# Performance work log

Measured on AMD Instinct MI355X. Metric: run time of the kernel, lower is better.

Reference implementation:

```python
import jax, jax.numpy as jnp
import numpy as np

N_SUPPORT = 8192
N_QUERY = 8192
INPUT_DIM = 1024
EMBED_DIM = 512
N_CLASSES = 64


def setup_inputs() -> dict:
    key = jax.random.key(0)
    k1, k2, k3, k4 = jax.random.split(key, 4)
    support_data = jax.random.normal(k1, (N_SUPPORT, INPUT_DIM), dtype=jnp.float32)
    query_data = jax.random.normal(k2, (N_QUERY, INPUT_DIM), dtype=jnp.float32)
    support_labels = jax.random.randint(k3, (N_SUPPORT,), 0, N_CLASSES, dtype=jnp.int32)
    W = jax.random.normal(k4, (INPUT_DIM, EMBED_DIM), dtype=jnp.float32) * (1.0 / np.sqrt(INPUT_DIM))
    return {"support_data": support_data, "support_labels": support_labels,
            "query_data": query_data, "W": W}


def _l2_normalize(x, eps=1e-12):
    # Matches F.normalize(p=2): x / max(||x||, eps)
    n = jnp.linalg.norm(x, axis=-1, keepdims=True)
    return x / jnp.maximum(n, eps)


def reference(support_data, support_labels, query_data, W):
    # encoder: single linear projection
    s_emb = support_data @ W            # [Ns, D]
    q_emb = query_data @ W              # [Nq, D]
    s_norm = _l2_normalize(s_emb)
    q_norm = _l2_normalize(q_emb)
    # cosine similarities for all query/support pairs: [Nq, Ns]
    sims = q_norm @ s_norm.T
    # per-class sum over support samples (torch.unique -> sorted 0..N_CLASSES-1)
    # segment_sum along the support axis: [N_classes, Nq] -> [Nq, N_classes]
    class_scores = jax.ops.segment_sum(sims.T, support_labels, num_segments=N_CLASSES).T
    return jax.nn.softmax(class_scores, axis=-1)
```

## Files before the change

### kernel.cpp

```cpp
#include <hip/hip_runtime.h>
#include <hip/hip_bf16.h>

#define NS 8192
#define NQ 8192
#define NTOT 16384
#define KDIM 1024
#define ED 512
#define NC 64

typedef __attribute__((ext_vector_type(4))) float fx4;
typedef __attribute__((ext_vector_type(8))) short sx8;
typedef __attribute__((ext_vector_type(8))) unsigned short ux8;

__device__ __forceinline__ unsigned short f2bf(float f) {
  union { float f; unsigned u; } v; v.f = f;
  unsigned r = v.u + 0x7fffu + ((v.u >> 16) & 1u);
  return (unsigned short)(r >> 16);
}
__device__ __forceinline__ float bf2f(unsigned short h) {
  union { unsigned u; float f; } v; v.u = ((unsigned)h) << 16;
  return v.f;
}

__global__ __launch_bounds__(256) void k_prep(
    const float* __restrict__ W, unsigned short* __restrict__ Wtp,
    float* __restrict__ rowssq, float* __restrict__ Pacc) {
  int c = blockIdx.x * 256 + threadIdx.x;
  int lane = c & 63;
  int j    = (c >> 6) & 3;
  int s2   = (c >> 8) & 1;
  int kt   = (c >> 9) & 15;
  int n64  = c >> 13;
  int quad = lane >> 4, ml = lane & 15;
  int n  = n64 * 64 + j * 16 + ml;
  int kb = kt * 64 + (s2 * 4 + quad) * 8;
  ux8 o;
#pragma unroll
  for (int e = 0; e < 8; ++e) o[e] = f2bf(W[(size_t)(kb + e) * ED + n]);
  *(ux8*)&Wtp[(size_t)c * 8] = o;
  if (c < NTOT) rowssq[c] = 0.f;
  if (c < NC * ED) Pacc[c] = 0.f;
}

__global__ __launch_bounds__(256, 4) void k_gemm_embed(
    const float* __restrict__ Xs, const float* __restrict__ Xq,
    const unsigned short* __restrict__ Wtp,
    unsigned short* __restrict__ emb, float* __restrict__ rowssq) {
  __shared__ unsigned short Ash[2][64 * 8 * 8];

  int lid = blockIdx.x;
  int x = lid & 7;
  int s = lid >> 3;
  int m_blk = x * 32 + (s >> 2);
  int n_blk = s & 3;

  const float* Xsrc = (m_blk < 128)
      ? (Xs + (size_t)m_blk * 64 * KDIM)
      : (Xq + (size_t)(m_blk - 128) * 64 * KDIM);

  int t = threadIdx.x;
  int lane = t & 63, w = t >> 6;
  int quad = lane >> 4, ml = lane & 15;
  int n64 = n_blk * 2 + (w >> 1);
  int jb = (w & 1) * 2;

  const unsigned short* Bbase = Wtp + ((size_t)n64 * 8192 + lane) * 8;

  fx4 acc[4][2];
#pragma unroll
  for (int i = 0; i < 4; ++i)
#pragma unroll
    for (int j = 0; j < 2; ++j) acc[i][j] = fx4{0.f, 0.f, 0.f, 0.f};

  fx4 avA[2][2], avB[2][2];

  auto loadA = [&](int kt, fx4 (&av)[2][2]) {
    int k0 = kt * 64;
#pragma unroll
    for (int c = 0; c < 2; ++c) {
      int ch = t + 256 * c;
      int m = ch >> 3, kq = ch & 7;
      const float* g = &Xsrc[(size_t)m * KDIM + k0 + kq * 8];
      av[c][0] = *(const fx4*)g;
      av[c][1] = *(const fx4*)(g + 4);
    }
  };
  auto writeA = [&](const fx4 (&av)[2][2], int bbuf) {
#pragma unroll
    for (int c = 0; c < 2; ++c) {
      int ch = t + 256 * c;
      int m = ch >> 3, kq = ch & 7;
      ux8 o;
      o[0] = f2bf(av[c][0].x); o[1] = f2bf(av[c][0].y);
      o[2] = f2bf(av[c][0].z); o[3] = f2bf(av[c][0].w);
      o[4] = f2bf(av[c][1].x); o[5] = f2bf(av[c][1].y);
      o[6] = f2bf(av[c][1].z); o[7] = f2bf(av[c][1].w);
      *(ux8*)&Ash[bbuf][((m * 8) + (kq ^ (m & 7))) * 8] = o;
    }
  };
  auto loadB = [&](int kt, sx8 (&bf)[2][2]) {
#pragma unroll
    for (int s2 = 0; s2 < 2; ++s2)
#pragma unroll
      for (int j = 0; j < 2; ++j)
        bf[s2][j] = *(const sx8*)&Bbase[(size_t)(kt * 512 + s2 * 256 + (jb + j) * 64) * 8];
  };
  auto compute = [&](int b, const sx8 (&bf)[2][2]) {
#pragma unroll
    for (int s2 = 0; s2 < 2; ++s2) {
      int kq = s2 * 4 + quad;
      sx8 af[4];
#pragma unroll
      for (int i = 0; i < 4; ++i) {
        int row = i * 16 + ml;
        af[i] = *(const sx8*)&Ash[b][(row * 8 + (kq ^ (row & 7))) * 8];
      }
#pragma unroll
      for (int i = 0; i < 4; ++i)
#pragma unroll
        for (int j = 0; j < 2; ++j)
          acc[i][j] = __builtin_amdgcn_mfma_f32_16x16x32_bf16(af[i], bf[s2][j], acc[i][j], 0, 0, 0);
    }
  };
  auto sync_step = [&]() {
    __builtin_amdgcn_sched_barrier(0);
    asm volatile("s_waitcnt lgkmcnt(0)" ::: "memory");
    __builtin_amdgcn_s_barrier();
    __builtin_amdgcn_sched_barrier(0);
  };

  loadA(0, avA);
  loadA(1, avB);
  writeA(avA, 0);
  sync_step();

  for (int it = 0; it < 8; ++it) {
    int kt0 = it * 2;
    sx8 bf[2][2];
    loadB(kt0, bf);
    loadA(kt0 + 2 < 16 ? kt0 + 2 : 15, avA);
    compute(0, bf);
    writeA(avB, 1);
    sync_step();

    loadB(kt0 + 1, bf);
    loadA(kt0 + 3 < 16 ? kt0 + 3 : 15, avB);
    compute(1, bf);
    writeA(avA, 0);
    sync_step();
  }

  int grow = m_blk * 64;
  int gcol = n_blk * 128 + w * 32;
#pragma unroll
  for (int i = 0; i < 4; ++i) {
#pragma unroll
    for (int r = 0; r < 4; ++r) {
      int mrow = grow + i * 16 + quad * 4 + r;
      float p = 0.f;
#pragma unroll
      for (int j = 0; j < 2; ++j) {
        emb[(size_t)mrow * ED + gcol + j * 16 + ml] = f2bf(acc[i][j][r]);
        p += acc[i][j][r] * acc[i][j][r];
      }
#pragma unroll
      for (int off = 1; off < 16; off <<= 1) p += __shfl_xor(p, off, 16);
      if (ml == 0) atomicAdd(&rowssq[mrow], p);
    }
  }
}

__global__ __launch_bounds__(256) void k_proto(
    const unsigned short* __restrict__ embS, const float* __restrict__ rowssq,
    const int* __restrict__ labels, float* __restrict__ Pacc) {
  __shared__ float Pl[NC * 64];
  int t = threadIdx.x;
#pragma unroll
  for (int i = 0; i < 16; ++i) Pl[i * 256 + t] = 0.f;
  __syncthreads();

  int w = t >> 6, lane = t & 63;
  int ds = blockIdx.y;
  int row0 = blockIdx.x * 256;
#pragma unroll 4
  for (int r = w; r < 256; r += 4) {
    int row = row0 + r;
    int lbl = labels[row];
    float scale = 1.0f / fmaxf(sqrtf(rowssq[row]), 1e-12f);
    float v = bf2f(embS[(size_t)row * ED + ds * 64 + lane]) * scale;
    atomicAdd(&Pl[lbl * 64 + lane], v);
  }
  __syncthreads();

#pragma unroll
  for (int i = 0; i < 16; ++i) {
    int idx = i * 256 + t;
    atomicAdd(&Pacc[(size_t)(idx >> 6) * ED + ds * 64 + (idx & 63)], Pl[idx]);
  }
}

__global__ __launch_bounds__(64) void k_scores(
    const unsigned short* __restrict__ embQ, const float* __restrict__ ssqQ,
    const float* __restrict__ Pacc, float* __restrict__ out) {
  int lane = threadIdx.x;
  int quad = lane >> 4, ml = lane & 15;
  int qrow0 = blockIdx.x * 16;

  fx4 acc[4];
#pragma unroll
  for (int i = 0; i < 4; ++i) acc[i] = fx4{0.f, 0.f, 0.f, 0.f};

#pragma unroll 4
  for (int ki = 0; ki < 16; ++ki) {
    sx8 a = *(const sx8*)&embQ[(size_t)(qrow0 + ml) * ED + ki * 32 + quad * 8];
    int d0 = ki * 32 + quad * 8;
#pragma unroll
    for (int nt = 0; nt < 4; ++nt) {
      const float* Prow = &Pacc[(size_t)(nt * 16 + ml) * ED + d0];
      fx4 p0 = *(const fx4*)Prow;
      fx4 p1 = *(const fx4*)(Prow + 4);
      ux8 bb;
      bb[0] = f2bf(p0.x); bb[1] = f2bf(p0.y); bb[2] = f2bf(p0.z); bb[3] = f2bf(p0.w);
      bb[4] = f2bf(p1.x); bb[5] = f2bf(p1.y); bb[6] = f2bf(p1.z); bb[7] = f2bf(p1.w);
      acc[nt] = __builtin_amdgcn_mfma_f32_16x16x32_bf16(a, *(sx8*)&bb, acc[nt], 0, 0, 0);
    }
  }

#pragma unroll
  for (int r = 0; r < 4; ++r) {
    int qq = qrow0 + quad * 4 + r;
    float scale = 1.0f / fmaxf(sqrtf(ssqQ[qq]), 1e-12f);
    float s[4];
#pragma unroll
    for (int nt = 0; nt < 4; ++nt) s[nt] = acc[nt][r] * scale;
    float m = fmaxf(fmaxf(s[0], s[1]), fmaxf(s[2], s[3]));
#pragma unroll
    for (int off = 1; off < 16; off <<= 1) m = fmaxf(m, __shfl_xor(m, off, 16));
    float e[4], ssum = 0.f;
#pragma unroll
    for (int nt = 0; nt < 4; ++nt) { e[nt] = __expf(s[nt] - m); ssum += e[nt]; }
#pragma unroll
    for (int off = 1; off < 16; off <<= 1) ssum += __shfl_xor(ssum, off, 16);
    float inv = 1.0f / ssum;
#pragma unroll
    for (int nt = 0; nt < 4; ++nt)
      out[(size_t)qq * NC + nt * 16 + ml] = e[nt] * inv;
  }
}

extern "C" void kernel_launch(void* const* d_in, const int* in_sizes, int n_in,
                              void* d_out, int out_size, void* d_ws, size_t ws_size,
                              hipStream_t stream) {
  const float* Xs     = (const float*)d_in[0];
  const int*   labels = (const int*)d_in[1];
  const float* Xq     = (const float*)d_in[2];
  const float* W      = (const float*)d_in[3];
  float* out = (float*)d_out;

  char* ws = (char*)d_ws;
  size_t off = 0;
  unsigned short* Wtp = (unsigned short*)(ws + off); off += (size_t)ED * KDIM * 2;
  unsigned short* emb = (unsigned short*)(ws + off); off += (size_t)NTOT * ED * 2;
  float* rowssq = (float*)(ws + off); off += (size_t)NTOT * 4;
  float* Pacc   = (float*)(ws + off); off += (size_t)NC * ED * 4;

  k_prep<<<256, 256, 0, stream>>>(W, Wtp, rowssq, Pacc);
  k_gemm_embed<<<1024, 256, 0, stream>>>(Xs, Xq, Wtp, emb, rowssq);
  k_proto<<<dim3(32, 8), 256, 0, stream>>>(emb, rowssq, labels, Pacc);
  k_scores<<<NQ / 16, 64, 0, stream>>>(emb + (size_t)NS * ED, rowssq + NS, Pacc, out);
}
```

Before: 173.4 us.

## Prefetch B fragments one step ahead and stage bf16 prototypes in LDS

The embedding GEMM now double-buffers the W fragments in registers, loading the next k-tile's B operands before computing the current one so their global latency overlaps the MFMAs. The scores kernel grows to 256-thread blocks of 64 queries. Each block converts the fp32 prototype matrix to bf16 once into a 64 KB shared-memory layout, so waves no longer reload and reconvert it from global memory for every query tile. The costs are extra VGPRs in the GEMM and heavy LDS use in the scores kernel, which can limit occupancy.

```diff
diff --git a/kernel.cpp b/kernel.cpp
--- a/kernel.cpp
+++ b/kernel.cpp
@@ -73,6 +73,7 @@
     for (int j = 0; j < 2; ++j) acc[i][j] = fx4{0.f, 0.f, 0.f, 0.f};
 
   fx4 avA[2][2], avB[2][2];
+  sx8 bfA[2][2], bfB[2][2];
 
   auto loadA = [&](int kt, fx4 (&av)[2][2]) {
     int k0 = kt * 64;
@@ -129,6 +130,7 @@
     __builtin_amdgcn_sched_barrier(0);
   };
 
+  loadB(0, bfA);
   loadA(0, avA);
   loadA(1, avB);
   writeA(avA, 0);
@@ -136,16 +138,15 @@
 
   for (int it = 0; it < 8; ++it) {
     int kt0 = it * 2;
-    sx8 bf[2][2];
-    loadB(kt0, bf);
+    loadB(kt0 + 1, bfB);
     loadA(kt0 + 2 < 16 ? kt0 + 2 : 15, avA);
-    compute(0, bf);
+    compute(0, bfA);
     writeA(avB, 1);
     sync_step();
 
-    loadB(kt0 + 1, bf);
+    loadB(kt0 + 2 < 16 ? kt0 + 2 : 15, bfA);
     loadA(kt0 + 3 < 16 ? kt0 + 3 : 15, avB);
-    compute(1, bf);
+    compute(1, bfB);
     writeA(avA, 0);
     sync_step();
   }
@@ -199,12 +200,28 @@
   }
 }
 
-__global__ __launch_bounds__(64) void k_scores(
+__global__ __launch_bounds__(256) void k_scores(
     const unsigned short* __restrict__ embQ, const float* __restrict__ ssqQ,
     const float* __restrict__ Pacc, float* __restrict__ out) {
-  int lane = threadIdx.x;
+  __shared__ unsigned short Pl[4096 * 8];
+  int t = threadIdx.x;
+#pragma unroll
+  for (int i = 0; i < 16; ++i) {
+    int c = t + 256 * i;
+    int cls = c & 63, ks = c >> 6;
+    const float* p = &Pacc[(size_t)cls * ED + ks * 8];
+    fx4 p0 = *(const fx4*)p;
+    fx4 p1 = *(const fx4*)(p + 4);
+    ux8 bb;
+    bb[0] = f2bf(p0.x); bb[1] = f2bf(p0.y); bb[2] = f2bf(p0.z); bb[3] = f2bf(p0.w);
+    bb[4] = f2bf(p1.x); bb[5] = f2bf(p1.y); bb[6] = f2bf(p1.z); bb[7] = f2bf(p1.w);
+    *(ux8*)&Pl[(size_t)c * 8] = bb;
+  }
+  __syncthreads();
+
+  int w = t >> 6, lane = t & 63;
   int quad = lane >> 4, ml = lane & 15;
-  int qrow0 = blockIdx.x * 16;
+  int qrow0 = blockIdx.x * 64 + w * 16;
 
   fx4 acc[4];
 #pragma unroll
@@ -213,16 +230,10 @@
 #pragma unroll 4
   for (int ki = 0; ki < 16; ++ki) {
     sx8 a = *(const sx8*)&embQ[(size_t)(qrow0 + ml) * ED + ki * 32 + quad * 8];
-    int d0 = ki * 32 + quad * 8;
 #pragma unroll
     for (int nt = 0; nt < 4; ++nt) {
-      const float* Prow = &Pacc[(size_t)(nt * 16 + ml) * ED + d0];
-      fx4 p0 = *(const fx4*)Prow;
-      fx4 p1 = *(const fx4*)(Prow + 4);
-      ux8 bb;
-      bb[0] = f2bf(p0.x); bb[1] = f2bf(p0.y); bb[2] = f2bf(p0.z); bb[3] = f2bf(p0.w);
-      bb[4] = f2bf(p1.x); bb[5] = f2bf(p1.y); bb[6] = f2bf(p1.z); bb[7] = f2bf(p1.w);
-      acc[nt] = __builtin_amdgcn_mfma_f32_16x16x32_bf16(a, *(sx8*)&bb, acc[nt], 0, 0, 0);
+      sx8 b = *(const sx8*)&Pl[((ki * 4 + quad) * 64 + nt * 16 + ml) * 8];
+      acc[nt] = __builtin_amdgcn_mfma_f32_16x16x32_bf16(a, b, acc[nt], 0, 0, 0);
     }
   }
 
@@ -267,5 +278,5 @@
   k_prep<<<256, 256, 0, stream>>>(W, Wtp, rowssq, Pacc);
   k_gemm_embed<<<1024, 256, 0, stream>>>(Xs, Xq, Wtp, emb, rowssq);
   k_proto<<<dim3(32, 8), 256, 0, stream>>>(emb, rowssq, labels, Pacc);
-  k_scores<<<NQ / 16, 64, 0, stream>>>(emb + (size_t)NS * ED, rowssq + NS, Pacc, out);
-}
+  k_scores<<<NQ / 64, 256, 0, stream>>>(emb + (size_t)NS * ED, rowssq + NS, Pacc, out);
+}
```

New measurement: 174.1 us. Within noise of the previous version (+0.4%).
